# Performance work log

Hardware: AMD Instinct MI355X
Metric: run time of the kernel (lower is better)

Reference implementation:

```python
import jax, jax.numpy as jnp
import numpy as np

EPS = 1e-5

def setup_inputs() -> dict:
    key = jax.random.key(0)
    k1, k2, k3, k4, k5 = jax.random.split(key, 5)
    B, N, K, HW, C = 2, 128, 64, 65536, 134
    # class probabilities (rows need not be normalized for the matcher math)
    input_class_prob = jax.random.uniform(k1, (B, N, C), dtype=jnp.float32)
    # predicted mask probabilities in [0, 1]
    input_mask = jax.random.uniform(k2, (B, N, HW), dtype=jnp.float32)
    # binary ground-truth masks (stored as float32 for the reduction math)
    target_mask = (jax.random.uniform(k3, (B, K, HW)) > 0.7).astype(jnp.float32)
    target_class = jax.random.randint(k4, (B, K), 0, C, dtype=jnp.int64)
    target_sizes = jax.random.randint(k5, (B,), 1, K + 1, dtype=jnp.int64)
    return {
        "input_class_prob": input_class_prob,
        "input_mask": input_mask,
        "target_mask": target_mask,
        "target_class": target_class,
        "target_sizes": target_sizes,
    }


def reference(input_class_prob, input_mask, target_mask, target_class, target_sizes):
    """Similarity-matrix stage of HungarianMatcher.

    Returns sim: (B, N, K) = sim_class * sim_dice.
    The subsequent scipy linear_sum_assignment is CPU-only with
    data-dependent shapes and is excluded from the kernelizable math.
    """
    B, N, _ = input_class_prob.shape
    K = target_class.shape[-1]
    # sim_class[b, n, k] = input_class_prob[b, n, target_class[b, k]]
    idx = jnp.broadcast_to(target_class[:, None, :], (B, N, K))
    sim_class = jnp.take_along_axis(input_class_prob, idx, axis=-1)
    # dice similarity without materializing the (B, N, K, HW) broadcast:
    # intersections via GEMM, cardinalities via row/col sums + broadcast.
    intersections = jnp.einsum("bnp,bkp->bnk", input_mask, target_mask)
    cardinalities = input_mask.sum(-1)[:, :, None] + target_mask.sum(-1)[:, None, :]
    sim_dice = (2.0 * intersections + EPS) / (cardinalities + EPS)
    return sim_class * sim_dice
```

## Files before the change

### kernel.cpp

```cpp
#include <hip/hip_runtime.h>

#define HWX 65536
#define NQ 128
#define KT 64
#define CC 134
#define BB 2
#define NW 128
#define WIN 512
#define SUB 64
#define NSUB 8
#define EPSI 1e-5f

typedef __attribute__((ext_vector_type(4))) float f32x4;
typedef __attribute__((ext_vector_type(8))) short bf16x8;

union FU { unsigned int u[4]; bf16x8 v; };

static __device__ __forceinline__ unsigned int cvtpk(float lo, float hi) {
  unsigned int r;
  asm("v_cvt_pk_bf16_f32 %0, %1, %2" : "=v"(r) : "v"(lo), "v"(hi));
  return r;
}

static __device__ __forceinline__ void gload16(const float* g, float* l) {
  __builtin_amdgcn_global_load_lds(
      (const __attribute__((address_space(1))) void*)g,
      (__attribute__((address_space(3))) void*)l, 16, 0, 0);
}

#define STAGE_SYNC()                                           \
  do {                                                         \
    asm volatile("s_waitcnt vmcnt(0)" ::: "memory");           \
    __syncthreads();                                           \
  } while (0)

__global__ void hm_detect(const unsigned int* __restrict__ t,
                          unsigned int* __restrict__ flag) {
  unsigned int w = t[threadIdx.x * 2 + 1];
  unsigned long long any = __ballot(w != 0u);
  if (threadIdx.x == 0) *flag = (any != 0ull) ? 1u : 0u;
}

template <bool ATOMIC>
__global__ __launch_bounds__(512)
void hm_stage1(const float* __restrict__ in_mask, const float* __restrict__ tg_mask,
               float* __restrict__ Ipart, float* __restrict__ RSin,
               float* __restrict__ RStg) {
  const int w = blockIdx.x & (NW - 1);
  const int b = blockIdx.x >> 7;
  const int tid = threadIdx.x;
  const int lane = tid & 63;
  const int wv = tid >> 6;
  const int l16 = lane & 15;
  const int lg = lane >> 4;

  __shared__ __align__(16) float lA[2][128 * SUB];
  __shared__ __align__(16) float lB[2][64 * SUB];

  const float* Ab = in_mask + (size_t)b * NQ * HWX + (size_t)w * WIN;
  const float* Bb = tg_mask + (size_t)b * KT * HWX + (size_t)w * WIN;

  f32x4 acc[4];
  #pragma unroll
  for (int i = 0; i < 4; ++i) acc[i] = f32x4{0.f, 0.f, 0.f, 0.f};
  float rsA = 0.f;
  float rsB = 0.f;

  auto STAGE = [&](int t, int buf) {
    #pragma unroll
    for (int q = 0; q < 4; ++q) {
      const int r0 = wv * 16 + q * 4;
      const int row = r0 + (lane >> 4);
      const int csrc = (lane & 15) ^ (row & 7);
      gload16(Ab + (size_t)row * HWX + t * SUB + csrc * 4, &lA[buf][r0 * SUB]);
    }
    #pragma unroll
    for (int q = 0; q < 2; ++q) {
      const int r0 = wv * 8 + q * 4;
      const int row = r0 + (lane >> 4);
      const int csrc = (lane & 15) ^ (row & 7);
      gload16(Bb + (size_t)row * HWX + t * SUB + csrc * 4, &lB[buf][r0 * SUB]);
    }
  };

  auto COMP = [&](int buf) {
    const float* A32 = lA[buf];
    const float* B32 = lB[buf];
    const int xA = l16 & 7;
    const int Ra = wv * 16 + l16;
    #pragma unroll
    for (int s = 0; s < 2; ++s) {
      const int g0 = s * 8 + lg * 2;
      f32x4 alo = *(const f32x4*)(A32 + Ra * SUB + ((g0 ^ xA) << 2));
      f32x4 ahi = *(const f32x4*)(A32 + Ra * SUB + (((g0 + 1) ^ xA) << 2));
      rsA += (alo.x + alo.y) + (alo.z + alo.w) + (ahi.x + ahi.y) + (ahi.z + ahi.w);
      FU fa;
      fa.u[0] = cvtpk(alo.x, alo.y); fa.u[1] = cvtpk(alo.z, alo.w);
      fa.u[2] = cvtpk(ahi.x, ahi.y); fa.u[3] = cvtpk(ahi.z, ahi.w);
      #pragma unroll
      for (int cf = 0; cf < 4; ++cf) {
        const int Rb = cf * 16 + l16;
        f32x4 blo = *(const f32x4*)(B32 + Rb * SUB + ((g0 ^ xA) << 2));
        f32x4 bhi = *(const f32x4*)(B32 + Rb * SUB + (((g0 + 1) ^ xA) << 2));
        if (cf == wv)
          rsB += (blo.x + blo.y) + (blo.z + blo.w) + (bhi.x + bhi.y) + (bhi.z + bhi.w);
        FU fb;
        fb.u[0] = cvtpk(blo.x, blo.y); fb.u[1] = cvtpk(blo.z, blo.w);
        fb.u[2] = cvtpk(bhi.x, bhi.y); fb.u[3] = cvtpk(bhi.z, bhi.w);
        acc[cf] = __builtin_amdgcn_mfma_f32_16x16x32_bf16(fa.v, fb.v, acc[cf], 0, 0, 0);
      }
    }
  };

  STAGE(0, 0);
  STAGE_SYNC();
  #pragma unroll
  for (int t = 0; t < NSUB; ++t) {
    if (t + 1 < NSUB) STAGE(t + 1, (t + 1) & 1);
    COMP(t & 1);
    STAGE_SYNC();
  }

  #pragma unroll
  for (int cf = 0; cf < 4; ++cf) {
    #pragma unroll
    for (int j = 0; j < 4; ++j) {
      const int row = wv * 16 + lg * 4 + j;
      const int col = cf * 16 + l16;
      if (!ATOMIC)
        Ipart[((size_t)(b * NW + w) * NQ + row) * KT + col] = acc[cf][j];
      else
        atomicAdd(&Ipart[((size_t)b * NQ + row) * KT + col], acc[cf][j]);
    }
  }

  rsA += __shfl_xor(rsA, 16); rsA += __shfl_xor(rsA, 32);
  rsB += __shfl_xor(rsB, 16); rsB += __shfl_xor(rsB, 32);
  if (lg == 0) {
    const int row = wv * 16 + l16;
    if (!ATOMIC) RSin[(size_t)(b * NW + w) * NQ + row] = rsA;
    else         atomicAdd(&RSin[b * NQ + row], rsA);
    if (wv < 4) {
      if (!ATOMIC) RStg[(size_t)(b * NW + w) * KT + row] = rsB;
      else         atomicAdd(&RStg[b * KT + row], rsB);
    }
  }
}

__global__ __launch_bounds__(256)
void hm_stage2(const float* __restrict__ cprob, const void* __restrict__ tcls,
               const float* __restrict__ Ipart, const float* __restrict__ RSin,
               const float* __restrict__ RStg, float* __restrict__ out) {
  const int bn = blockIdx.x;
  const int b = bn >> 7, n = bn & 127;
  const int k = threadIdx.x & 63;
  const int wq = threadIdx.x >> 6;
  float I = 0.f, ra = 0.f, rg = 0.f;
  #pragma unroll 8
  for (int ww = 0; ww < NW / 4; ++ww) {
    const int w = wq * (NW / 4) + ww;
    I  += Ipart[((size_t)(b * NW + w) * NQ + n) * KT + k];
    ra += RSin[(size_t)(b * NW + w) * NQ + n];
    rg += RStg[(size_t)(b * NW + w) * KT + k];
  }
  __shared__ float sI[4][64];
  __shared__ float sG[4][64];
  __shared__ float sR[4];
  sI[wq][k] = I;
  sG[wq][k] = rg;
  if (k == 0) sR[wq] = ra;
  __syncthreads();
  if (wq == 0) {
    I  = sI[0][k] + sI[1][k] + sI[2][k] + sI[3][k];
    rg = sG[0][k] + sG[1][k] + sG[2][k] + sG[3][k];
    ra = sR[0] + sR[1] + sR[2] + sR[3];
    const unsigned int hiw = ((const unsigned int*)tcls)[k * 2 + 1];
    const bool i32 = (__ballot(hiw != 0u) != 0ull);
    int tc = i32 ? ((const int*)tcls)[b * KT + k]
                 : (int)((const long long*)tcls)[b * KT + k];
    const float c = cprob[((size_t)b * NQ + n) * CC + tc];
    out[(size_t)bn * KT + k] = c * (2.f * I + EPSI) / (ra + rg + EPSI);
  }
}

__global__ __launch_bounds__(256)
void hm_stage2_direct(const float* __restrict__ cprob, const void* __restrict__ tcls,
                      const unsigned int* __restrict__ flag,
                      const float* __restrict__ Iacc, const float* __restrict__ RSin,
                      const float* __restrict__ RStg, float* __restrict__ out) {
  const int idx = blockIdx.x * 256 + threadIdx.x;
  const int k = idx & 63;
  const int n = (idx >> 6) & 127;
  const int b = idx >> 13;
  const float I  = Iacc[idx];
  const float ra = RSin[b * NQ + n];
  const float rg = RStg[b * KT + k];
  int tc;
  if (*flag) tc = ((const int*)tcls)[b * KT + k];
  else       tc = (int)((const long long*)tcls)[b * KT + k];
  const float c = cprob[((size_t)b * NQ + n) * CC + tc];
  out[idx] = c * (2.f * I + EPSI) / (ra + rg + EPSI);
}

__global__ void hm_zero(float* __restrict__ p, int n) {
  int i = blockIdx.x * blockDim.x + threadIdx.x;
  if (i < n) p[i] = 0.f;
}

extern "C" void kernel_launch(void* const* d_in, const int* in_sizes, int n_in,
                              void* d_out, int out_size, void* d_ws, size_t ws_size,
                              hipStream_t stream) {
  const float* cprob = (const float*)d_in[0];
  const float* imask = (const float*)d_in[1];
  const float* tmask = (const float*)d_in[2];
  const void*  tcls  = d_in[3];
  float* out = (float*)d_out;

  const size_t ipart_f = (size_t)BB * NW * NQ * KT;
  const size_t rsin_f  = (size_t)BB * NW * NQ;
  const size_t rstg_f  = (size_t)BB * NW * KT;
  const size_t need    = (ipart_f + rsin_f + rstg_f) * sizeof(float);

  char* ws = (char*)d_ws;
  if (ws_size >= need) {
    float* Ipart = (float*)ws;
    float* RSin  = Ipart + ipart_f;
    float* RStg  = RSin + rsin_f;
    hm_stage1<false><<<BB * NW, 512, 0, stream>>>(imask, tmask, Ipart, RSin, RStg);
    hm_stage2<<<BB * NQ, 256, 0, stream>>>(cprob, tcls, Ipart, RSin, RStg, out);
  } else {
    float* Iacc = (float*)ws;
    float* RSin = Iacc + (size_t)BB * NQ * KT;
    float* RStg = RSin + BB * NQ;
    unsigned int* flag = (unsigned int*)(RStg + BB * KT);
    const int zn = BB * NQ * KT + BB * NQ + BB * KT;
    hm_zero<<<(zn + 255) / 256, 256, 0, stream>>>(Iacc, zn);
    hm_detect<<<1, 64, 0, stream>>>((const unsigned int*)tcls, flag);
    hm_stage1<true><<<BB * NW, 512, 0, stream>>>(imask, tmask, Iacc, RSin, RStg);
    hm_stage2_direct<<<(BB * NQ * KT) / 256, 256, 0, stream>>>(cprob, tcls, flag, Iacc, RSin, RStg, out);
  }
}
```

Before: 27.82 us.

## Preload target mask window once as bf16 and use per-wave A buffers without block barriers

Stage1 now loads the block's whole target-mask window (64 rows x 512 columns) into LDS once at the start. It converts it to bf16 with swizzling and computes the target row sums there, instead of reloading and re-converting B every subtile in every wave. Each wave now streams only its own 16 rows of the input mask into private double buffers, so the per-iteration __syncthreads is replaced by a vmcnt wait plus a sched barrier. This removes redundant B conversion work and block-wide syncs. The cost is a serialized B prologue and the loss of overlap between B loads and compute.

```diff
diff --git a/kernel.cpp b/kernel.cpp
--- a/kernel.cpp
+++ b/kernel.cpp
@@ -13,6 +13,7 @@
 
 typedef __attribute__((ext_vector_type(4))) float f32x4;
 typedef __attribute__((ext_vector_type(8))) short bf16x8;
+typedef __attribute__((ext_vector_type(2))) unsigned int u32x2;
 
 union FU { unsigned int u[4]; bf16x8 v; };
 
@@ -27,12 +28,6 @@
       (const __attribute__((address_space(1))) void*)g,
       (__attribute__((address_space(3))) void*)l, 16, 0, 0);
 }
-
-#define STAGE_SYNC()                                           \
-  do {                                                         \
-    asm volatile("s_waitcnt vmcnt(0)" ::: "memory");           \
-    __syncthreads();                                           \
-  } while (0)
 
 __global__ void hm_detect(const unsigned int* __restrict__ t,
                           unsigned int* __restrict__ flag) {
@@ -54,8 +49,8 @@
   const int l16 = lane & 15;
   const int lg = lane >> 4;
 
-  __shared__ __align__(16) float lA[2][128 * SUB];
-  __shared__ __align__(16) float lB[2][64 * SUB];
+  __shared__ __align__(16) unsigned short lB[64 * 512];
+  __shared__ __align__(16) float lA[8][2][16 * SUB];
 
   const float* Ab = in_mask + (size_t)b * NQ * HWX + (size_t)w * WIN;
   const float* Bb = tg_mask + (size_t)b * KT * HWX + (size_t)w * WIN;
@@ -64,61 +59,75 @@
   #pragma unroll
   for (int i = 0; i < 4; ++i) acc[i] = f32x4{0.f, 0.f, 0.f, 0.f};
   float rsA = 0.f;
-  float rsB = 0.f;
-
-  auto STAGE = [&](int t, int buf) {
+
+  auto ISSUE_A = [&](int t, int buf) {
+    float* dst = &lA[wv][buf][0];
     #pragma unroll
     for (int q = 0; q < 4; ++q) {
-      const int r0 = wv * 16 + q * 4;
-      const int row = r0 + (lane >> 4);
+      const int row = q * 4 + (lane >> 4);
       const int csrc = (lane & 15) ^ (row & 7);
-      gload16(Ab + (size_t)row * HWX + t * SUB + csrc * 4, &lA[buf][r0 * SUB]);
-    }
-    #pragma unroll
-    for (int q = 0; q < 2; ++q) {
-      const int r0 = wv * 8 + q * 4;
-      const int row = r0 + (lane >> 4);
-      const int csrc = (lane & 15) ^ (row & 7);
-      gload16(Bb + (size_t)row * HWX + t * SUB + csrc * 4, &lB[buf][r0 * SUB]);
+      gload16(Ab + (size_t)(wv * 16 + row) * HWX + t * SUB + csrc * 4,
+              dst + q * 256);
     }
   };
 
-  auto COMP = [&](int buf) {
-    const float* A32 = lA[buf];
-    const float* B32 = lB[buf];
-    const int xA = l16 & 7;
-    const int Ra = wv * 16 + l16;
+  ISSUE_A(0, 0);
+  {
+    const int brow = tid >> 3;
+    const int bl = tid & 7;
+    float rsB = 0.f;
+    char* B8 = (char*)lB;
+    #pragma unroll
+    for (int j = 0; j < 16; ++j) {
+      const int c = bl + j * 8;
+      f32x4 x = *(const f32x4*)(Bb + (size_t)brow * HWX + c * 4);
+      rsB += (x.x + x.y) + (x.z + x.w);
+      u32x2 v;
+      v.x = cvtpk(x.x, x.y); v.y = cvtpk(x.z, x.w);
+      const int ch16 = c >> 1, half = c & 1;
+      *(u32x2*)(B8 + (size_t)brow * 1024 +
+                (((ch16 ^ (brow & 7)) << 4) + half * 8)) = v;
+    }
+    rsB += __shfl_xor(rsB, 1); rsB += __shfl_xor(rsB, 2); rsB += __shfl_xor(rsB, 4);
+    if (bl == 0) {
+      if (!ATOMIC) RStg[(size_t)(b * NW + w) * KT + brow] = rsB;
+      else         atomicAdd(&RStg[b * KT + brow], rsB);
+    }
+  }
+  asm volatile("s_waitcnt vmcnt(0)" ::: "memory");
+  __syncthreads();
+
+  auto COMP = [&](int t, int buf) {
+    const float* A32 = &lA[wv][buf][0];
+    const char* B8 = (const char*)lB;
+    const int x7 = l16 & 7;
     #pragma unroll
     for (int s = 0; s < 2; ++s) {
       const int g0 = s * 8 + lg * 2;
-      f32x4 alo = *(const f32x4*)(A32 + Ra * SUB + ((g0 ^ xA) << 2));
-      f32x4 ahi = *(const f32x4*)(A32 + Ra * SUB + (((g0 + 1) ^ xA) << 2));
+      f32x4 alo = *(const f32x4*)(A32 + l16 * SUB + ((g0 ^ x7) << 2));
+      f32x4 ahi = *(const f32x4*)(A32 + l16 * SUB + (((g0 + 1) ^ x7) << 2));
       rsA += (alo.x + alo.y) + (alo.z + alo.w) + (ahi.x + ahi.y) + (ahi.z + ahi.w);
       FU fa;
       fa.u[0] = cvtpk(alo.x, alo.y); fa.u[1] = cvtpk(alo.z, alo.w);
       fa.u[2] = cvtpk(ahi.x, ahi.y); fa.u[3] = cvtpk(ahi.z, ahi.w);
+      const int c16 = t * 8 + s * 4 + lg;
       #pragma unroll
       for (int cf = 0; cf < 4; ++cf) {
         const int Rb = cf * 16 + l16;
-        f32x4 blo = *(const f32x4*)(B32 + Rb * SUB + ((g0 ^ xA) << 2));
-        f32x4 bhi = *(const f32x4*)(B32 + Rb * SUB + (((g0 + 1) ^ xA) << 2));
-        if (cf == wv)
-          rsB += (blo.x + blo.y) + (blo.z + blo.w) + (bhi.x + bhi.y) + (bhi.z + bhi.w);
-        FU fb;
-        fb.u[0] = cvtpk(blo.x, blo.y); fb.u[1] = cvtpk(blo.z, blo.w);
-        fb.u[2] = cvtpk(bhi.x, bhi.y); fb.u[3] = cvtpk(bhi.z, bhi.w);
-        acc[cf] = __builtin_amdgcn_mfma_f32_16x16x32_bf16(fa.v, fb.v, acc[cf], 0, 0, 0);
+        bf16x8 fbv = *(const bf16x8*)(B8 + (size_t)Rb * 1024 +
+                                      ((c16 ^ (Rb & 7)) << 4));
+        acc[cf] = __builtin_amdgcn_mfma_f32_16x16x32_bf16(fa.v, fbv, acc[cf], 0, 0, 0);
       }
     }
   };
 
-  STAGE(0, 0);
-  STAGE_SYNC();
   #pragma unroll
   for (int t = 0; t < NSUB; ++t) {
-    if (t + 1 < NSUB) STAGE(t + 1, (t + 1) & 1);
-    COMP(t & 1);
-    STAGE_SYNC();
+    const int buf = t & 1;
+    if (t + 1 < NSUB) ISSUE_A(t + 1, buf ^ 1);
+    COMP(t, buf);
+    asm volatile("s_waitcnt vmcnt(0)" ::: "memory");
+    __builtin_amdgcn_sched_barrier(0);
   }
 
   #pragma unroll
@@ -135,15 +144,10 @@
   }
 
   rsA += __shfl_xor(rsA, 16); rsA += __shfl_xor(rsA, 32);
-  rsB += __shfl_xor(rsB, 16); rsB += __shfl_xor(rsB, 32);
   if (lg == 0) {
     const int row = wv * 16 + l16;
     if (!ATOMIC) RSin[(size_t)(b * NW + w) * NQ + row] = rsA;
     else         atomicAdd(&RSin[b * NQ + row], rsA);
-    if (wv < 4) {
-      if (!ATOMIC) RStg[(size_t)(b * NW + w) * KT + row] = rsB;
-      else         atomicAdd(&RStg[b * KT + row], rsB);
-    }
   }
 }
 
```

New measurement: 26.25 us. -5.6%, faster.
